# Kernel tuning notes

Measured on AMD Instinct MI355X. Metric: run time of the kernel, lower is better.

Reference implementation:

```python
import jax, jax.numpy as jnp
import numpy as np

ALPHA = 0.2          # LeakyReLU negative slope
NEG_INF = -9e15      # mask value used by the original module
B, L, D, F_IN, F_OUT = 16, 256, 128, 64, 64


def setup_inputs() -> dict:
    key = jax.random.key(0)
    k1, k2, k3, k4 = jax.random.split(key, 4)
    h = jax.random.normal(k1, (B, L, D, F_IN), dtype=jnp.float32)
    adj = jax.random.randint(k2, (B, L, D, D), 0, 2, dtype=jnp.int32)
    # xavier_uniform(gain=1.414) bounds
    bW = 1.414 * np.sqrt(6.0 / (F_IN + F_OUT))
    W = jax.random.uniform(k3, (F_IN, F_OUT), dtype=jnp.float32, minval=-bW, maxval=bW)
    ba = 1.414 * np.sqrt(6.0 / (2 * F_OUT + 1))
    a = jax.random.uniform(k4, (2 * F_OUT, 1), dtype=jnp.float32, minval=-ba, maxval=ba)
    return {"h": h, "adj": adj, "W": W, "a": a}


def reference(h, adj, W, a):
    # h: [B,L,D,F_in], adj: [B,L,D,D]
    Wh = jnp.einsum('bldf,fo->bldo', h, W)              # [B,L,D,F_out]
    a1 = a[:F_OUT, 0]                                    # dots the "source" node i
    a2 = a[F_OUT:, 0]                                    # dots the "target" node j
    e_i = Wh @ a1                                        # [B,L,D]
    e_j = Wh @ a2                                        # [B,L,D]
    e = e_i[..., :, None] + e_j[..., None, :]            # [B,L,D,D] pairwise scores
    e = jnp.where(e > 0, e, ALPHA * e)                   # LeakyReLU
    att = jnp.where(adj > 0, e, NEG_INF)
    att = jax.nn.softmax(att, axis=-1)                   # dropout=eval mode (no-op)
    h_prime = jnp.einsum('bldk,blko->bldo', att, Wh)     # [B,L,D,F_out]
    return h_prime
```

## Files before the change

### kernel.cpp

```cpp
#include <hip/hip_runtime.h>

constexpr int D_   = 128;
constexpr int FIN  = 64;
constexpr int FOUT = 64;
constexpr float ALPHA = 0.2f;
constexpr int HT_S = 136;

static __device__ __forceinline__ unsigned short f2bf(float x) {
    unsigned u = __float_as_uint(x);
    unsigned r = (u + 0x7fffu + ((u >> 16) & 1u)) >> 16;
    return (unsigned short)r;
}
static __device__ __forceinline__ unsigned pack2(float a, float b) {
    return (unsigned)f2bf(a) | ((unsigned)f2bf(b) << 16);
}
#define BFLO(u) __uint_as_float((u) << 16)
#define BFHI(u) __uint_as_float((u) & 0xffff0000u)

__global__ __launch_bounds__(256, 4) void gat_kernel(
    const float* __restrict__ hg, const int* __restrict__ adjg,
    const float* __restrict__ Wg, const float* __restrict__ ag,
    float* __restrict__ outg)
{
    __shared__ unsigned short sHT[FIN * HT_S];
    __shared__ float sP[32 * 128];
    __shared__ float sEi[D_], sEj[D_], sL[D_];
    __shared__ float sA[2 * FOUT];

    const int tid = threadIdx.x;
    const long bl = blockIdx.x;
    const float* hp   = hg   + bl * (long)(D_ * FIN);
    const int*   adjp = adjg + bl * (long)(D_ * D_);
    float*       outp = outg + bl * (long)(D_ * FOUT);

    {
        const float4* W4 = (const float4*)Wg;
        float4* sW4 = (float4*)sP;
        #pragma unroll
        for (int k = 0; k < 4; ++k) sW4[tid + 256 * k] = W4[tid + 256 * k];
        if (tid < 2 * FOUT) sA[tid] = ag[tid];
        const float4* h4 = (const float4*)hp;
        #pragma unroll
        for (int k = 0; k < 8; ++k) {
            int idx = tid + 256 * k;
            float4 v = h4[idx];
            int row = idx >> 4;
            int f   = (idx & 15) << 2;
            sHT[(f + 0) * HT_S + row] = f2bf(v.x);
            sHT[(f + 1) * HT_S + row] = f2bf(v.y);
            sHT[(f + 2) * HT_S + row] = f2bf(v.z);
            sHT[(f + 3) * HT_S + row] = f2bf(v.w);
        }
    }
    __syncthreads();

    const int rg = tid >> 3;
    const int cg = tid & 7;
    float acc[4][8];
    #pragma unroll
    for (int r = 0; r < 4; ++r)
        #pragma unroll
        for (int c = 0; c < 8; ++c) acc[r][c] = 0.f;

    for (int f = 0; f < FIN; ++f) {
        uint2 hraw = *(const uint2*)&sHT[f * HT_S + rg * 4];
        float hr[4] = { BFLO(hraw.x), BFHI(hraw.x), BFLO(hraw.y), BFHI(hraw.y) };
        float4 w0 = *(const float4*)&sP[f * 64 + cg * 8];
        float4 w1 = *(const float4*)&sP[f * 64 + cg * 8 + 4];
        float wc[8] = {w0.x, w0.y, w0.z, w0.w, w1.x, w1.y, w1.z, w1.w};
        #pragma unroll
        for (int r = 0; r < 4; ++r)
            #pragma unroll
            for (int c = 0; c < 8; ++c)
                acc[r][c] += hr[r] * wc[c];
    }
    __syncthreads();

    #pragma unroll
    for (int r = 0; r < 4; ++r) {
        uint4 u;
        u.x = pack2(acc[r][0], acc[r][1]);
        u.y = pack2(acc[r][2], acc[r][3]);
        u.z = pack2(acc[r][4], acc[r][5]);
        u.w = pack2(acc[r][6], acc[r][7]);
        *(uint4*)&sHT[(rg * 4 + r) * 64 + cg * 8] = u;
    }
    __syncthreads();

    if (tid < D_) {
        float ei = 0.f, ej = 0.f;
        #pragma unroll
        for (int q = 0; q < 8; ++q) {
            uint4 wv = *(const uint4*)&sHT[tid * 64 + q * 8];
            float w0 = BFLO(wv.x), w1 = BFHI(wv.x), w2 = BFLO(wv.y), w3 = BFHI(wv.y);
            float w4 = BFLO(wv.z), w5 = BFHI(wv.z), w6 = BFLO(wv.w), w7 = BFHI(wv.w);
            float4 c1a = *(const float4*)&sA[q * 8];
            float4 c1b = *(const float4*)&sA[q * 8 + 4];
            float4 c2a = *(const float4*)&sA[FOUT + q * 8];
            float4 c2b = *(const float4*)&sA[FOUT + q * 8 + 4];
            ei += w0 * c1a.x + w1 * c1a.y + w2 * c1a.z + w3 * c1a.w
                + w4 * c1b.x + w5 * c1b.y + w6 * c1b.z + w7 * c1b.w;
            ej += w0 * c2a.x + w1 * c2a.y + w2 * c2a.z + w3 * c2a.w
                + w4 * c2b.x + w5 * c2b.y + w6 * c2b.z + w7 * c2b.w;
        }
        sEi[tid] = ei;
        sEj[tid] = ej;
        sL[tid]  = 0.f;
    }
    __syncthreads();

    #pragma unroll
    for (int r = 0; r < 4; ++r)
        #pragma unroll
        for (int c = 0; c < 8; ++c) acc[r][c] = 0.f;

    const int pi = tid >> 1;
    const int pjb = (tid & 1) << 4;

    for (int t4 = 0; t4 < 4; ++t4) {
        const int j0 = t4 * 32;
        {
            const float ei = sEi[pi];
            float lp = 0.f;
            const int4* arow = (const int4*)&adjp[pi * D_ + j0 + pjb];
            #pragma unroll
            for (int q = 0; q < 4; ++q) {
                int4 av = arow[q];
                int aa[4] = {av.x, av.y, av.z, av.w};
                #pragma unroll
                for (int k = 0; k < 4; ++k) {
                    int j = pjb + q * 4 + k;
                    float e = ei + sEj[j0 + j];
                    e = e > 0.f ? e : ALPHA * e;
                    float p = (aa[k] > 0) ? __expf(e) : 0.f;
                    sP[j * 128 + pi] = p;
                    lp += p;
                }
            }
            lp += __shfl_xor(lp, 1);
            if ((tid & 1) == 0) sL[pi] += lp;
        }
        __syncthreads();
        for (int jj = 0; jj < 32; ++jj) {
            uint4 wr = *(const uint4*)&sHT[(j0 + jj) * 64 + cg * 8];
            float wc[8] = { BFLO(wr.x), BFHI(wr.x), BFLO(wr.y), BFHI(wr.y),
                            BFLO(wr.z), BFHI(wr.z), BFLO(wr.w), BFHI(wr.w) };
            float4 pv = *(const float4*)&sP[jj * 128 + rg * 4];
            float pr[4] = {pv.x, pv.y, pv.z, pv.w};
            #pragma unroll
            for (int r = 0; r < 4; ++r)
                #pragma unroll
                for (int c = 0; c < 8; ++c)
                    acc[r][c] += pr[r] * wc[c];
        }
        __syncthreads();
    }

    #pragma unroll
    for (int r = 0; r < 4; ++r) {
        float inv = 1.0f / sL[rg * 4 + r];
        float4 v0 = make_float4(acc[r][0] * inv, acc[r][1] * inv,
                                acc[r][2] * inv, acc[r][3] * inv);
        float4 v1 = make_float4(acc[r][4] * inv, acc[r][5] * inv,
                                acc[r][6] * inv, acc[r][7] * inv);
        *(float4*)&outp[(rg * 4 + r) * 64 + cg * 8]     = v0;
        *(float4*)&outp[(rg * 4 + r) * 64 + cg * 8 + 4] = v1;
    }
}

extern "C" void kernel_launch(void* const* d_in, const int* in_sizes, int n_in,
                              void* d_out, int out_size, void* d_ws, size_t ws_size,
                              hipStream_t stream) {
    const float* h   = (const float*)d_in[0];
    const int*   adj = (const int*)d_in[1];
    const float* W   = (const float*)d_in[2];
    const float* a   = (const float*)d_in[3];
    float*       out = (float*)d_out;
    gat_kernel<<<dim3(16 * 256), dim3(256), 0, stream>>>(h, adj, W, a, out);
}
```

Baseline: 544.5 us.

## Use fp16 MFMA for both matmuls with swizzled LDS and register-prefetched adjacency

Moves the projection h·W and the attention-weighted aggregation P·Wh from scalar FMAs onto MFMA 16x16x32 f16 instructions. Operands are stored in XOR-swizzled LDS layouts to avoid bank conflicts. The e_i/e_j scores are now computed from the MFMA accumulators with wave shuffles, and a per-block max subtraction is added for the softmax. Adjacency tiles are prefetched into registers one tile ahead, and bf16 storage is replaced with fp16, which carries some risk of overflow or precision loss.

```diff
diff --git a/kernel.cpp b/kernel.cpp
--- a/kernel.cpp
+++ b/kernel.cpp
@@ -4,41 +4,41 @@
 constexpr int FIN  = 64;
 constexpr int FOUT = 64;
 constexpr float ALPHA = 0.2f;
-constexpr int HT_S = 136;
-
-static __device__ __forceinline__ unsigned short f2bf(float x) {
-    unsigned u = __float_as_uint(x);
-    unsigned r = (u + 0x7fffu + ((u >> 16) & 1u)) >> 16;
-    return (unsigned short)r;
-}
-static __device__ __forceinline__ unsigned pack2(float a, float b) {
-    return (unsigned)f2bf(a) | ((unsigned)f2bf(b) << 16);
-}
-#define BFLO(u) __uint_as_float((u) << 16)
-#define BFHI(u) __uint_as_float((u) & 0xffff0000u)
+
+typedef _Float16 f16x8 __attribute__((ext_vector_type(8)));
+typedef float    f32x4 __attribute__((ext_vector_type(4)));
 
 __global__ __launch_bounds__(256, 4) void gat_kernel(
     const float* __restrict__ hg, const int* __restrict__ adjg,
     const float* __restrict__ Wg, const float* __restrict__ ag,
     float* __restrict__ outg)
 {
-    __shared__ unsigned short sHT[FIN * HT_S];
-    __shared__ float sP[32 * 128];
-    __shared__ float sEi[D_], sEj[D_], sL[D_];
-    __shared__ float sA[2 * FOUT];
-
-    const int tid = threadIdx.x;
+    __shared__ __align__(16) unsigned short sX[128 * 64];
+    __shared__ __align__(16) unsigned short sPt[64 * 64];
+    __shared__ __align__(16) float sA[2 * FOUT];
+    __shared__ float sEi[D_];
+    __shared__ __align__(16) float sEj[D_];
+    __shared__ float sL[D_];
+    __shared__ float sMxW[4];
+
+    const int tid  = threadIdx.x;
+    const int lane = tid & 63;
+    const int w    = tid >> 6;
+    const int g    = lane >> 4;
+    const int m16  = lane & 15;
+
     const long bl = blockIdx.x;
     const float* hp   = hg   + bl * (long)(D_ * FIN);
     const int*   adjp = adjg + bl * (long)(D_ * D_);
     float*       outp = outg + bl * (long)(D_ * FOUT);
 
+    char* xb = (char*)sX;
+    char* pb = (char*)sPt;
+
+    const int pi  = tid >> 1;
+    const int pjb = (tid & 1) << 4;
+
     {
-        const float4* W4 = (const float4*)Wg;
-        float4* sW4 = (float4*)sP;
-        #pragma unroll
-        for (int k = 0; k < 4; ++k) sW4[tid + 256 * k] = W4[tid + 256 * k];
-        if (tid < 2 * FOUT) sA[tid] = ag[tid];
         const float4* h4 = (const float4*)hp;
         #pragma unroll
         for (int k = 0; k < 8; ++k) {
@@ -46,125 +46,192 @@
             float4 v = h4[idx];
             int row = idx >> 4;
             int f   = (idx & 15) << 2;
-            sHT[(f + 0) * HT_S + row] = f2bf(v.x);
-            sHT[(f + 1) * HT_S + row] = f2bf(v.y);
-            sHT[(f + 2) * HT_S + row] = f2bf(v.z);
-            sHT[(f + 3) * HT_S + row] = f2bf(v.w);
-        }
+            union { _Float16 h[4]; uint2 u; } cv;
+            cv.h[0] = (_Float16)v.x; cv.h[1] = (_Float16)v.y;
+            cv.h[2] = (_Float16)v.z; cv.h[3] = (_Float16)v.w;
+            int off = (row * 128 + f * 2) ^ ((row & 7) << 4);
+            *(uint2*)(xb + off) = cv.u;
+        }
+        const float4* W4 = (const float4*)Wg;
+        #pragma unroll
+        for (int k = 0; k < 4; ++k) {
+            int idx = tid + 256 * k;
+            float4 v = W4[idx];
+            int f  = idx >> 4;
+            int o0 = (idx & 15) << 2;
+            float vv[4] = {v.x, v.y, v.z, v.w};
+            #pragma unroll
+            for (int q = 0; q < 4; ++q) {
+                int o = o0 + q;
+                int off = (o * 128 + f * 2) ^ ((o & 7) << 4);
+                *(_Float16*)(pb + off) = (_Float16)vv[q];
+            }
+        }
+        if (tid < 2 * FOUT) sA[tid] = ag[tid];
+    }
+
+    int4 areg[4];
+    {
+        const int4* ap = (const int4*)(adjp + pi * D_ + pjb);
+        #pragma unroll
+        for (int q = 0; q < 4; ++q) areg[q] = ap[q];
     }
     __syncthreads();
 
-    const int rg = tid >> 3;
-    const int cg = tid & 7;
-    float acc[4][8];
-    #pragma unroll
-    for (int r = 0; r < 4; ++r)
-        #pragma unroll
-        for (int c = 0; c < 8; ++c) acc[r][c] = 0.f;
-
-    for (int f = 0; f < FIN; ++f) {
-        uint2 hraw = *(const uint2*)&sHT[f * HT_S + rg * 4];
-        float hr[4] = { BFLO(hraw.x), BFHI(hraw.x), BFLO(hraw.y), BFHI(hraw.y) };
-        float4 w0 = *(const float4*)&sP[f * 64 + cg * 8];
-        float4 w1 = *(const float4*)&sP[f * 64 + cg * 8 + 4];
-        float wc[8] = {w0.x, w0.y, w0.z, w0.w, w1.x, w1.y, w1.z, w1.w};
-        #pragma unroll
-        for (int r = 0; r < 4; ++r)
-            #pragma unroll
-            for (int c = 0; c < 8; ++c)
-                acc[r][c] += hr[r] * wc[c];
+    f32x4 acc[2][4];
+    #pragma unroll
+    for (int mt = 0; mt < 2; ++mt)
+        #pragma unroll
+        for (int nt = 0; nt < 4; ++nt) acc[mt][nt] = (f32x4){0.f, 0.f, 0.f, 0.f};
+
+    #pragma unroll
+    for (int kt = 0; kt < 2; ++kt) {
+        f16x8 af[2], bf[4];
+        #pragma unroll
+        for (int mt = 0; mt < 2; ++mt) {
+            int row = w * 32 + mt * 16 + m16;
+            af[mt] = *(const f16x8*)(xb + ((row * 128 + kt * 64 + g * 16) ^ ((row & 7) << 4)));
+        }
+        #pragma unroll
+        for (int nt = 0; nt < 4; ++nt) {
+            int o = nt * 16 + m16;
+            bf[nt] = *(const f16x8*)(pb + ((o * 128 + kt * 64 + g * 16) ^ ((o & 7) << 4)));
+        }
+        #pragma unroll
+        for (int mt = 0; mt < 2; ++mt)
+            #pragma unroll
+            for (int nt = 0; nt < 4; ++nt)
+                acc[mt][nt] = __builtin_amdgcn_mfma_f32_16x16x32_f16(af[mt], bf[nt], acc[mt][nt], 0, 0, 0);
     }
     __syncthreads();
 
-    #pragma unroll
-    for (int r = 0; r < 4; ++r) {
-        uint4 u;
-        u.x = pack2(acc[r][0], acc[r][1]);
-        u.y = pack2(acc[r][2], acc[r][3]);
-        u.z = pack2(acc[r][4], acc[r][5]);
-        u.w = pack2(acc[r][6], acc[r][7]);
-        *(uint4*)&sHT[(rg * 4 + r) * 64 + cg * 8] = u;
+    {
+        float a1v[4], a2v[4];
+        #pragma unroll
+        for (int nt = 0; nt < 4; ++nt) {
+            a1v[nt] = sA[nt * 16 + m16];
+            a2v[nt] = sA[FOUT + nt * 16 + m16];
+        }
+        float wmax = -3.0e38f;
+        #pragma unroll
+        for (int mt = 0; mt < 2; ++mt) {
+            #pragma unroll
+            for (int r = 0; r < 4; ++r) {
+                float ei = 0.f, ej = 0.f;
+                #pragma unroll
+                for (int nt = 0; nt < 4; ++nt) {
+                    float v = acc[mt][nt][r];
+                    ei += v * a1v[nt];
+                    ej += v * a2v[nt];
+                }
+                #pragma unroll
+                for (int s = 1; s < 16; s <<= 1) {
+                    ei += __shfl_xor(ei, s);
+                    ej += __shfl_xor(ej, s);
+                }
+                int row = w * 32 + mt * 16 + g * 4 + r;
+                if (m16 == 0) { sEi[row] = ei; sEj[row] = ej; }
+                wmax = fmaxf(wmax, ej);
+            }
+        }
+        wmax = fmaxf(wmax, __shfl_xor(wmax, 16));
+        wmax = fmaxf(wmax, __shfl_xor(wmax, 32));
+        if (lane == 0) sMxW[w] = wmax;
+
+        #pragma unroll
+        for (int mt = 0; mt < 2; ++mt) {
+            int j0r = w * 32 + mt * 16 + g * 4;
+            #pragma unroll
+            for (int nt = 0; nt < 4; ++nt) {
+                int o = nt * 16 + m16;
+                union { _Float16 h[4]; uint2 u; } cv;
+                cv.h[0] = (_Float16)acc[mt][nt][0];
+                cv.h[1] = (_Float16)acc[mt][nt][1];
+                cv.h[2] = (_Float16)acc[mt][nt][2];
+                cv.h[3] = (_Float16)acc[mt][nt][3];
+                int off = (o * 256 + j0r * 2) ^ ((o & 7) << 4);
+                *(uint2*)(xb + off) = cv.u;
+            }
+        }
     }
     __syncthreads();
 
-    if (tid < D_) {
-        float ei = 0.f, ej = 0.f;
-        #pragma unroll
-        for (int q = 0; q < 8; ++q) {
-            uint4 wv = *(const uint4*)&sHT[tid * 64 + q * 8];
-            float w0 = BFLO(wv.x), w1 = BFHI(wv.x), w2 = BFLO(wv.y), w3 = BFHI(wv.y);
-            float w4 = BFLO(wv.z), w5 = BFHI(wv.z), w6 = BFLO(wv.w), w7 = BFHI(wv.w);
-            float4 c1a = *(const float4*)&sA[q * 8];
-            float4 c1b = *(const float4*)&sA[q * 8 + 4];
-            float4 c2a = *(const float4*)&sA[FOUT + q * 8];
-            float4 c2b = *(const float4*)&sA[FOUT + q * 8 + 4];
-            ei += w0 * c1a.x + w1 * c1a.y + w2 * c1a.z + w3 * c1a.w
-                + w4 * c1b.x + w5 * c1b.y + w6 * c1b.z + w7 * c1b.w;
-            ej += w0 * c2a.x + w1 * c2a.y + w2 * c2a.z + w3 * c2a.w
-                + w4 * c2b.x + w5 * c2b.y + w6 * c2b.z + w7 * c2b.w;
-        }
-        sEi[tid] = ei;
-        sEj[tid] = ej;
-        sL[tid]  = 0.f;
-    }
-    __syncthreads();
-
-    #pragma unroll
-    for (int r = 0; r < 4; ++r)
-        #pragma unroll
-        for (int c = 0; c < 8; ++c) acc[r][c] = 0.f;
-
-    const int pi = tid >> 1;
-    const int pjb = (tid & 1) << 4;
-
-    for (int t4 = 0; t4 < 4; ++t4) {
-        const int j0 = t4 * 32;
+    #pragma unroll
+    for (int mt = 0; mt < 2; ++mt)
+        #pragma unroll
+        for (int nt = 0; nt < 4; ++nt) acc[mt][nt] = (f32x4){0.f, 0.f, 0.f, 0.f};
+
+    const float ei_pi = sEi[pi];
+    const float mxj = fmaxf(fmaxf(sMxW[0], sMxW[1]), fmaxf(sMxW[2], sMxW[3]));
+    float mt_ = ei_pi + mxj;
+    const float mi = mt_ > 0.f ? mt_ : ALPHA * mt_;
+    float lpt = 0.f;
+
+    for (int jt = 0; jt < 4; ++jt) {
+        const int j0 = jt * 32;
+        union { _Float16 h[8]; uint4 u; } ph0, ph1;
+        #pragma unroll
+        for (int q = 0; q < 4; ++q) {
+            int4 av = areg[q];
+            int aa[4] = {av.x, av.y, av.z, av.w};
+            float4 ej4 = *(const float4*)&sEj[j0 + pjb + q * 4];
+            float ejv[4] = {ej4.x, ej4.y, ej4.z, ej4.w};
+            #pragma unroll
+            for (int kk = 0; kk < 4; ++kk) {
+                float e = ei_pi + ejv[kk];
+                e = e > 0.f ? e : ALPHA * e;
+                float p = (aa[kk] > 0) ? __expf(e - mi) : 0.f;
+                lpt += p;
+                _Float16 pv = (_Float16)p;
+                if (q < 2) ph0.h[q * 4 + kk] = pv;
+                else       ph1.h[(q - 2) * 4 + kk] = pv;
+            }
+        }
         {
-            const float ei = sEi[pi];
-            float lp = 0.f;
-            const int4* arow = (const int4*)&adjp[pi * D_ + j0 + pjb];
-            #pragma unroll
-            for (int q = 0; q < 4; ++q) {
-                int4 av = arow[q];
-                int aa[4] = {av.x, av.y, av.z, av.w};
-                #pragma unroll
-                for (int k = 0; k < 4; ++k) {
-                    int j = pjb + q * 4 + k;
-                    float e = ei + sEj[j0 + j];
-                    e = e > 0.f ? e : ALPHA * e;
-                    float p = (aa[k] > 0) ? __expf(e) : 0.f;
-                    sP[j * 128 + pi] = p;
-                    lp += p;
-                }
-            }
-            lp += __shfl_xor(lp, 1);
-            if ((tid & 1) == 0) sL[pi] += lp;
+            int base = pi * 64 + pjb * 2;
+            *(uint4*)(pb + ((base)      ^ ((pi & 3) << 4))) = ph0.u;
+            *(uint4*)(pb + ((base + 16) ^ ((pi & 3) << 4))) = ph1.u;
+        }
+        if (jt < 3) {
+            const int4* ap = (const int4*)(adjp + pi * D_ + (jt + 1) * 32 + pjb);
+            #pragma unroll
+            for (int q = 0; q < 4; ++q) areg[q] = ap[q];
+        } else {
+            lpt += __shfl_xor(lpt, 1);
+            if ((tid & 1) == 0) sL[pi] = lpt;
         }
         __syncthreads();
-        for (int jj = 0; jj < 32; ++jj) {
-            uint4 wr = *(const uint4*)&sHT[(j0 + jj) * 64 + cg * 8];
-            float wc[8] = { BFLO(wr.x), BFHI(wr.x), BFLO(wr.y), BFHI(wr.y),
-                            BFLO(wr.z), BFHI(wr.z), BFLO(wr.w), BFHI(wr.w) };
-            float4 pv = *(const float4*)&sP[jj * 128 + rg * 4];
-            float pr[4] = {pv.x, pv.y, pv.z, pv.w};
-            #pragma unroll
-            for (int r = 0; r < 4; ++r)
-                #pragma unroll
-                for (int c = 0; c < 8; ++c)
-                    acc[r][c] += pr[r] * wc[c];
-        }
-        __syncthreads();
-    }
-
-    #pragma unroll
-    for (int r = 0; r < 4; ++r) {
-        float inv = 1.0f / sL[rg * 4 + r];
-        float4 v0 = make_float4(acc[r][0] * inv, acc[r][1] * inv,
-                                acc[r][2] * inv, acc[r][3] * inv);
-        float4 v1 = make_float4(acc[r][4] * inv, acc[r][5] * inv,
-                                acc[r][6] * inv, acc[r][7] * inv);
-        *(float4*)&outp[(rg * 4 + r) * 64 + cg * 8]     = v0;
-        *(float4*)&outp[(rg * 4 + r) * 64 + cg * 8 + 4] = v1;
+
+        f16x8 pa[2], wb[4];
+        #pragma unroll
+        for (int mtx = 0; mtx < 2; ++mtx) {
+            int i = w * 32 + mtx * 16 + m16;
+            pa[mtx] = *(const f16x8*)(pb + ((i * 64 + g * 16) ^ ((i & 3) << 4)));
+        }
+        #pragma unroll
+        for (int nt = 0; nt < 4; ++nt) {
+            int o = nt * 16 + m16;
+            wb[nt] = *(const f16x8*)(xb + ((o * 256 + j0 * 2 + g * 16) ^ ((o & 7) << 4)));
+        }
+        #pragma unroll
+        for (int mtx = 0; mtx < 2; ++mtx)
+            #pragma unroll
+            for (int nt = 0; nt < 4; ++nt)
+                acc[mtx][nt] = __builtin_amdgcn_mfma_f32_16x16x32_f16(pa[mtx], wb[nt], acc[mtx][nt], 0, 0, 0);
+
+        if (jt < 3) __syncthreads();
+    }
+
+    #pragma unroll
+    for (int mtx = 0; mtx < 2; ++mtx) {
+        #pragma unroll
+        for (int r = 0; r < 4; ++r) {
+            int row = w * 32 + mtx * 16 + g * 4 + r;
+            float inv = 1.0f / sL[row];
+            #pragma unroll
+            for (int nt = 0; nt < 4; ++nt)
+                outp[row * 64 + nt * 16 + m16] = acc[mtx][nt][r] * inv;
+        }
     }
 }
 
```

Measured after the change: 491.2 us. 9.8% less time.
